# Kernel optimization log

Measured on AMD Instinct MI355X. Metric: run time of the kernel, lower is better.

Reference implementation:

```python
import jax, jax.numpy as jnp
import numpy as np

WEIGHT_STD = 0.1
WEIGHT_STD2 = 2.0 * WEIGHT_STD ** 2  # 0.02
CONF_THRESH = 0.9


def setup_inputs() -> dict:
    key = jax.random.key(0)
    k0, k1, k2, k3 = jax.random.split(key, 4)
    B, N, V, J = 1, 32768, 10475, 55
    # skinning weights: nonnegative, rows sum to 1 (as in SMPL-X)
    lbs_weights = jax.random.uniform(k0, (V, J), dtype=jnp.float32)
    lbs_weights = lbs_weights / jnp.sum(lbs_weights, -1, keepdims=True)
    verts_transform = jax.random.normal(k1, (B, V, 4, 4), dtype=jnp.float32)
    points = jax.random.normal(k2, (B, N, 3), dtype=jnp.float32)
    template_points = jax.random.normal(k3, (B, V, 3), dtype=jnp.float32)
    return {
        "lbs_weights": lbs_weights,
        "verts_transform": verts_transform,
        "points": points,
        "template_points": template_points,
        "K": 6,
    }


def _knn(points, template_points, K):
    """Brute-force KNN; squared L2 dists like pytorch3d knn_points. -> dists, idx [B,N,K] ascending."""
    p2 = jnp.sum(points * points, -1)[:, :, None]            # [B,N,1]
    t2 = jnp.sum(template_points * template_points, -1)[:, None, :]  # [B,1,V]
    cross = jnp.einsum("bnd,bvd->bnv", points, template_points)     # [B,N,V]
    d2 = jnp.maximum(p2 + t2 - 2.0 * cross, 0.0)
    neg_d, idx = jax.lax.top_k(-d2, K)  # largest of -d2 == smallest d2, sorted ascending
    return -neg_d, idx


def reference(lbs_weights, verts_transform, points, template_points, K):
    B = points.shape[0]
    neighbs_dist, neighbs = _knn(points, template_points, K)  # [B,N,K]

    # gather skinning weights of the K neighbors: [B,N,K,J]
    w_n = lbs_weights[neighbs]
    # confidence: neighbors whose lbs weights agree with the nearest one
    conf = jnp.exp(-jnp.sum(jnp.abs(w_n - w_n[..., 0:1, :]), -1) / WEIGHT_STD2)
    conf = (conf > CONF_THRESH).astype(neighbs_dist.dtype)
    w = jnp.exp(-neighbs_dist) * conf
    w = w / jnp.sum(w, -1, keepdims=True)  # [B,N,K]; k=0 conf always 1 -> sum > 0

    # gather per-vertex 4x4 transforms: [B,N,K,4,4]
    vt_n = verts_transform[jnp.arange(B)[:, None, None], neighbs]
    xyz_transform = jnp.sum(w[..., None, None] * vt_n, axis=2)   # [B,N,4,4]
    xyz_dist = jnp.sum(w * neighbs_dist, axis=2, keepdims=True)  # [B,N,1]
    return xyz_dist, xyz_transform
```

## Files before the change

### kernel.cpp

```cpp
#include <hip/hip_runtime.h>
#include <math.h>

#pragma clang fp contract(off)

#define NPTS  32768
#define NV    10475
#define JW    55
#define TILE  512
#define NT    21
#define BLOCK 256
#define R     4
#define PPB   16
#define CAP   22
#define FINF  3.4e38f
#define GMARG 0.001f

#define FOR4(M) M(0) M(1) M(2) M(3)

#define LTL(dd, vv, D, I) ((dd) < (D) || ((dd) == (D) && (vv) < (I)))
#define INSL6(dd, vv, D0,I0,D1,I1,D2,I2,D3,I3,D4,I4,D5,I5) \
  if (LTL(dd, vv, D5, I5)) { \
    if (LTL(dd, vv, D4, I4)) { D5=D4; I5=I4; \
      if (LTL(dd, vv, D3, I3)) { D4=D3; I4=I3; \
        if (LTL(dd, vv, D2, I2)) { D3=D2; I3=I2; \
          if (LTL(dd, vv, D1, I1)) { D2=D1; I2=I1; \
            if (LTL(dd, vv, D0, I0)) { D1=D0; I1=I0; D0=(dd); I0=(vv); } \
            else { D1=(dd); I1=(vv); } \
          } else { D2=(dd); I2=(vv); } \
        } else { D3=(dd); I3=(vv); } \
      } else { D4=(dd); I4=(vv); } \
    } else { D5=(dd); I5=(vv); } \
  }

__global__ __launch_bounds__(BLOCK, 6)
void scarf_knn_lbs(const float* __restrict__ lbs,
                   const float* __restrict__ vtf,
                   const float* __restrict__ pts,
                   const float* __restrict__ tpl,
                   float* __restrict__ out_dist,
                   float* __restrict__ out_tf)
{
    __shared__ float4 s_tile[2][TILE];
    __shared__ float  s_bd[PPB][CAP];
    __shared__ int    s_bi[PPB][CAP];
    __shared__ int    s_cnt[PPB];
    __shared__ float  s_td[PPB][6];
    __shared__ int    s_ti[PPB][6];

    const int tid = threadIdx.x;
    const int h   = tid & 63;
    const int w   = tid >> 6;
    const int lp  = w * R;
    const int p0  = blockIdx.x * PPB + lp;

    if (tid < PPB) s_cnt[tid] = 0;

    #define DECLP(r) \
      const float Px##r = 2.0f * pts[(p0+(r))*3+0]; \
      const float Py##r = 2.0f * pts[(p0+(r))*3+1]; \
      const float Pz##r = 2.0f * pts[(p0+(r))*3+2]; \
      const float q##r  = (Px##r*Px##r + Py##r*Py##r) + Pz##r*Pz##r;
    FOR4(DECLP)

    float gx[2], gy[2], gz[2];
    #define STAGE_ISSUE(t_) { \
      _Pragma("unroll") \
      for (int k = 0; k < 2; ++k) { \
        const int j = (t_) * TILE + k * BLOCK + tid; \
        if (j < NV) { gx[k] = tpl[j*3+0]; gy[k] = tpl[j*3+1]; gz[k] = tpl[j*3+2]; } \
        else        { gx[k] = 1.0e6f;    gy[k] = 1.0e6f;    gz[k] = 1.0e6f;    } } }
    #define STAGE_WRITE(dst_) { \
      _Pragma("unroll") \
      for (int k = 0; k < 2; ++k) { \
        const float X = gx[k]+gx[k], Y = gy[k]+gy[k], Z = gz[k]+gz[k]; \
        s_tile[dst_][k * BLOCK + tid] = \
          make_float4(-(X+X), -(Y+Y), -(Z+Z), (X*X + Y*Y) + Z*Z); } }

    #define DECLM(r) float m##r = FINF;
    FOR4(DECLM)

    #define EVP1(r) { \
      const float da = fmaf(Pz##r, ta.z, fmaf(Py##r, ta.y, fmaf(Px##r, ta.x, ta.w))); \
      const float db = fmaf(Pz##r, tb.z, fmaf(Py##r, tb.y, fmaf(Px##r, tb.x, tb.w))); \
      m##r = fminf(fminf(m##r, da), db); }

    STAGE_ISSUE(0); STAGE_WRITE(0); __syncthreads();
    for (int t = 0; t < NT; ++t) {
        if (t + 1 < NT) STAGE_ISSUE(t + 1);
        const float4* bp = s_tile[t & 1];
        #pragma unroll
        for (int itp = 0; itp < 4; ++itp) {
            const float4 ta = bp[(2*itp    ) * 64 + h];
            const float4 tb = bp[(2*itp + 1) * 64 + h];
            FOR4(EVP1)
        }
        if (t + 1 < NT) { STAGE_WRITE((t + 1) & 1); __syncthreads(); }
    }

    #define DECLT(r) float G##r; { \
      float v = m##r; float M; \
      _Pragma("unroll") \
      for (int rep = 0; rep < 6; ++rep) { \
        M = v; \
        M = fminf(M, __shfl_xor(M, 1)); \
        M = fminf(M, __shfl_xor(M, 2)); \
        M = fminf(M, __shfl_xor(M, 4)); \
        M = fminf(M, __shfl_xor(M, 8)); \
        M = fminf(M, __shfl_xor(M, 16)); \
        M = fminf(M, __shfl_xor(M, 32)); \
        if (rep < 5) v = (v == M) ? FINF : v; \
      } \
      G##r = M + GMARG; }
    FOR4(DECLT)

    __syncthreads();

    #define EVP2(r) { \
      const float dp = fmaf(Pz##r, tv.z, fmaf(Py##r, tv.y, fmaf(Px##r, tv.x, tv.w))); \
      if (dp <= G##r) { \
        const float Xr = -0.5f * tv.x, Yr = -0.5f * tv.y, Zr = -0.5f * tv.z; \
        const float C  = fmaf(Pz##r, Zr, fmaf(Py##r, Yr, Px##r * Xr)); \
        const float de = fmaf(-2.0f, C, q##r + tv.w);   \
        const int k = atomicAdd(&s_cnt[lp+(r)], 1); \
        if (k < CAP) { s_bd[lp+(r)][k] = fmaxf(de, 0.0f); s_bi[lp+(r)][k] = tb + it*64 + h; } } }

    STAGE_ISSUE(0); STAGE_WRITE(0); __syncthreads();
    for (int t = 0; t < NT; ++t) {
        if (t + 1 < NT) STAGE_ISSUE(t + 1);
        const float4* bp = s_tile[t & 1];
        const int tb = t * TILE;
        #pragma unroll
        for (int it = 0; it < 8; ++it) {
            const float4 tv = bp[it * 64 + h];
            FOR4(EVP2)
        }
        if (t + 1 < NT) { STAGE_WRITE((t + 1) & 1); __syncthreads(); }
    }

    if (h < R) {
        const int lpr = lp + h;
        float D0=FINF,D1=FINF,D2=FINF,D3=FINF,D4=FINF,D5=FINF;
        int   I0=-1,I1=-1,I2=-1,I3=-1,I4=-1,I5=-1;
        const int cc = s_cnt[lpr];
        const int c  = (cc < CAP) ? cc : CAP;
        for (int k = 0; k < c; ++k) {
            const float dd = s_bd[lpr][k]; const int vv = s_bi[lpr][k];
            INSL6(dd, vv, D0,I0,D1,I1,D2,I2,D3,I3,D4,I4,D5,I5);
        }
        s_td[lpr][0]=D0; s_td[lpr][1]=D1; s_td[lpr][2]=D2;
        s_td[lpr][3]=D3; s_td[lpr][4]=D4; s_td[lpr][5]=D5;
        s_ti[lpr][0]=I0; s_ti[lpr][1]=I1; s_ti[lpr][2]=I2;
        s_ti[lpr][3]=I3; s_ti[lpr][4]=I4; s_ti[lpr][5]=I5;
    }

    const int r  = h >> 4;
    const int l  = h & 15;
    const int lpr = lp + r;
    const int i0 = s_ti[lpr][0];
    const int i1 = s_ti[lpr][1], i2 = s_ti[lpr][2], i3 = s_ti[lpr][3];
    const int i4 = s_ti[lpr][4], i5 = s_ti[lpr][5];
    {
        float s1 = 0.0f, s2 = 0.0f, s3 = 0.0f, s4 = 0.0f, s5 = 0.0f;
        for (int j = l; j < JW; j += 16) {
            const float w0 = lbs[(long)i0 * JW + j];
            s1 += fabsf(lbs[(long)i1 * JW + j] - w0);
            s2 += fabsf(lbs[(long)i2 * JW + j] - w0);
            s3 += fabsf(lbs[(long)i3 * JW + j] - w0);
            s4 += fabsf(lbs[(long)i4 * JW + j] - w0);
            s5 += fabsf(lbs[(long)i5 * JW + j] - w0);
        }
        s1 += __shfl_xor(s1,1); s1 += __shfl_xor(s1,2); s1 += __shfl_xor(s1,4); s1 += __shfl_xor(s1,8);
        s2 += __shfl_xor(s2,1); s2 += __shfl_xor(s2,2); s2 += __shfl_xor(s2,4); s2 += __shfl_xor(s2,8);
        s3 += __shfl_xor(s3,1); s3 += __shfl_xor(s3,2); s3 += __shfl_xor(s3,4); s3 += __shfl_xor(s3,8);
        s4 += __shfl_xor(s4,1); s4 += __shfl_xor(s4,2); s4 += __shfl_xor(s4,4); s4 += __shfl_xor(s4,8);
        s5 += __shfl_xor(s5,1); s5 += __shfl_xor(s5,2); s5 += __shfl_xor(s5,4); s5 += __shfl_xor(s5,8);
        const float sv = (l==0)?s1:(l==1)?s2:(l==2)?s3:(l==3)?s4:s5;
        const bool pred = (l < 5) && (expf(-sv / 0.02f) > 0.9f);
        const unsigned long long bal = __ballot(pred);
        const unsigned mr = (unsigned)(bal >> (r * 16)) & 31u;

        const int P = p0 + r;
        const float d0 = 0.25f * s_td[lpr][0], d1 = 0.25f * s_td[lpr][1];
        const float d2 = 0.25f * s_td[lpr][2], d3 = 0.25f * s_td[lpr][3];
        const float d4 = 0.25f * s_td[lpr][4], d5 = 0.25f * s_td[lpr][5];

        const float w0 = expf(-d0);
        const float w1 = (mr & 1u)  ? expf(-d1) : 0.0f;
        const float w2 = (mr & 2u)  ? expf(-d2) : 0.0f;
        const float w3 = (mr & 4u)  ? expf(-d3) : 0.0f;
        const float w4 = (mr & 8u)  ? expf(-d4) : 0.0f;
        const float w5 = (mr & 16u) ? expf(-d5) : 0.0f;
        const float inv = 1.0f / (w0 + w1 + w2 + w3 + w4 + w5);
        const float n0 = w0*inv, n1 = w1*inv, n2 = w2*inv;
        const float n3 = w3*inv, n4 = w4*inv, n5 = w5*inv;

        if (l == 0)
            out_dist[P] = n0*d0 + n1*d1 + n2*d2 + n3*d3 + n4*d4 + n5*d5;

        float acc = n0 * vtf[i0*16 + l];
        acc = fmaf(n1, vtf[i1*16 + l], acc);
        acc = fmaf(n2, vtf[i2*16 + l], acc);
        acc = fmaf(n3, vtf[i3*16 + l], acc);
        acc = fmaf(n4, vtf[i4*16 + l], acc);
        acc = fmaf(n5, vtf[i5*16 + l], acc);
        out_tf[P*16 + l] = acc;
    }
}

extern "C" void kernel_launch(void* const* d_in, const int* in_sizes, int n_in,
                              void* d_out, int out_size, void* d_ws, size_t ws_size,
                              hipStream_t stream) {
    const float* lbs = (const float*)d_in[0];
    const float* vtf = (const float*)d_in[1];
    const float* pts = (const float*)d_in[2];
    const float* tpl = (const float*)d_in[3];
    float* out = (float*)d_out;
    scarf_knn_lbs<<<NPTS / PPB, BLOCK, 0, stream>>>(lbs, vtf, pts, tpl, out, out + NPTS);
}
```

Baseline: 114.7 us.

## Fuse KNN threshold and collection passes using a progressively tightened bound

The separate full pass that found each point's exact 6th-nearest threshold is replaced by a short warm-up over the first 4 template tiles. A single collection pass then appends candidates under that bound while tracking running minima, and re-tightens the bound with wave shuffles every few tiles. This removes most of one full scan over all template vertices. In exchange the early bound is looser, so more candidates reach shared memory through atomics; the candidate cap is raised to 64. If a point still exceeds the cap, true neighbours seen later are dropped and the result is wrong.

```diff
diff --git a/kernel.cpp b/kernel.cpp
--- a/kernel.cpp
+++ b/kernel.cpp
@@ -8,10 +8,11 @@
 #define JW    55
 #define TILE  512
 #define NT    21
+#define NINIT 4
 #define BLOCK 256
 #define R     4
 #define PPB   16
-#define CAP   22
+#define CAP   64
 #define FINF  3.4e38f
 #define GMARG 0.001f
 
@@ -79,25 +80,29 @@
     #define DECLM(r) float m##r = FINF;
     FOR4(DECLM)
 
-    #define EVP1(r) { \
+    #define EVI(r) { \
       const float da = fmaf(Pz##r, ta.z, fmaf(Py##r, ta.y, fmaf(Px##r, ta.x, ta.w))); \
       const float db = fmaf(Pz##r, tb.z, fmaf(Py##r, tb.y, fmaf(Px##r, tb.x, tb.w))); \
       m##r = fminf(fminf(m##r, da), db); }
 
-    STAGE_ISSUE(0); STAGE_WRITE(0); __syncthreads();
-    for (int t = 0; t < NT; ++t) {
-        if (t + 1 < NT) STAGE_ISSUE(t + 1);
-        const float4* bp = s_tile[t & 1];
-        #pragma unroll
-        for (int itp = 0; itp < 4; ++itp) {
-            const float4 ta = bp[(2*itp    ) * 64 + h];
-            const float4 tb = bp[(2*itp + 1) * 64 + h];
-            FOR4(EVP1)
-        }
-        if (t + 1 < NT) { STAGE_WRITE((t + 1) & 1); __syncthreads(); }
-    }
-
-    #define DECLT(r) float G##r; { \
+    #define EVG(r) { \
+      const float da = fmaf(Pz##r, ta.z, fmaf(Py##r, ta.y, fmaf(Px##r, ta.x, ta.w))); \
+      const float db = fmaf(Pz##r, tb.z, fmaf(Py##r, tb.y, fmaf(Px##r, tb.x, tb.w))); \
+      if (da <= U##r) { \
+        const float Xr = -0.5f * ta.x, Yr = -0.5f * ta.y, Zr = -0.5f * ta.z; \
+        const float C  = fmaf(Pz##r, Zr, fmaf(Py##r, Yr, Px##r * Xr)); \
+        const float de = fmaf(-2.0f, C, q##r + ta.w); \
+        const int k = atomicAdd(&s_cnt[lp+(r)], 1); \
+        if (k < CAP) { s_bd[lp+(r)][k] = fmaxf(de, 0.0f); s_bi[lp+(r)][k] = ia; } } \
+      if (db <= U##r) { \
+        const float Xr = -0.5f * tb.x, Yr = -0.5f * tb.y, Zr = -0.5f * tb.z; \
+        const float C  = fmaf(Pz##r, Zr, fmaf(Py##r, Yr, Px##r * Xr)); \
+        const float de = fmaf(-2.0f, C, q##r + tb.w); \
+        const int k = atomicAdd(&s_cnt[lp+(r)], 1); \
+        if (k < CAP) { s_bd[lp+(r)][k] = fmaxf(de, 0.0f); s_bi[lp+(r)][k] = ib; } } \
+      m##r = fminf(fminf(m##r, da), db); }
+
+    #define UPDT(r) { \
       float v = m##r; float M; \
       _Pragma("unroll") \
       for (int rep = 0; rep < 6; ++rep) { \
@@ -110,31 +115,39 @@
         M = fminf(M, __shfl_xor(M, 32)); \
         if (rep < 5) v = (v == M) ? FINF : v; \
       } \
-      G##r = M + GMARG; }
-    FOR4(DECLT)
-
-    __syncthreads();
-
-    #define EVP2(r) { \
-      const float dp = fmaf(Pz##r, tv.z, fmaf(Py##r, tv.y, fmaf(Px##r, tv.x, tv.w))); \
-      if (dp <= G##r) { \
-        const float Xr = -0.5f * tv.x, Yr = -0.5f * tv.y, Zr = -0.5f * tv.z; \
-        const float C  = fmaf(Pz##r, Zr, fmaf(Py##r, Yr, Px##r * Xr)); \
-        const float de = fmaf(-2.0f, C, q##r + tv.w);   \
-        const int k = atomicAdd(&s_cnt[lp+(r)], 1); \
-        if (k < CAP) { s_bd[lp+(r)][k] = fmaxf(de, 0.0f); s_bi[lp+(r)][k] = tb + it*64 + h; } } }
+      U##r = M + GMARG; }
+
+    STAGE_ISSUE(0); STAGE_WRITE(0); __syncthreads();
+    for (int t = 0; t < NINIT; ++t) {
+        if (t + 1 < NINIT) STAGE_ISSUE(t + 1);
+        const float4* bp = s_tile[t & 1];
+        #pragma unroll
+        for (int itp = 0; itp < 4; ++itp) {
+            const float4 ta = bp[(2*itp    ) * 64 + h];
+            const float4 tb = bp[(2*itp + 1) * 64 + h];
+            FOR4(EVI)
+        }
+        if (t + 1 < NINIT) { STAGE_WRITE((t + 1) & 1); __syncthreads(); }
+    }
+
+    #define DECLU(r) float U##r; UPDT(r);
+    FOR4(DECLU)
 
     STAGE_ISSUE(0); STAGE_WRITE(0); __syncthreads();
     for (int t = 0; t < NT; ++t) {
         if (t + 1 < NT) STAGE_ISSUE(t + 1);
         const float4* bp = s_tile[t & 1];
-        const int tb = t * TILE;
+        const int tb0 = t * TILE;
         #pragma unroll
-        for (int it = 0; it < 8; ++it) {
-            const float4 tv = bp[it * 64 + h];
-            FOR4(EVP2)
+        for (int itp = 0; itp < 4; ++itp) {
+            const int ia = tb0 + (2*itp) * 64 + h;
+            const int ib = ia + 64;
+            const float4 ta = bp[(2*itp    ) * 64 + h];
+            const float4 tb = bp[(2*itp + 1) * 64 + h];
+            FOR4(EVG)
         }
         if (t + 1 < NT) { STAGE_WRITE((t + 1) & 1); __syncthreads(); }
+        if (t >= 4 && t % 3 == 1) { FOR4(UPDT) }
     }
 
     if (h < R) {
```

New measurement: 322.2 us. 181% more time.
